# Optimization experiments

Hardware: AMD Instinct MI355X
Metric: run time of the kernel (lower is better)

The kernel has to match this reference:

```python
import jax, jax.numpy as jnp
import numpy as np

N, E, D = 10000, 320000, 128
SIGMA = 0.3


def setup_inputs() -> dict:
    key = jax.random.key(0)
    ks = jax.random.split(key, 24)
    f32 = jnp.float32
    inp = {
        "h": jax.random.normal(ks[0], (N, D), f32),
        "e": jax.random.normal(ks[1], (E, D), f32),
        "p": jax.random.normal(ks[2], (N, D), f32),
        "d": jax.random.normal(ks[3], (N, D), f32),
        "dt": jax.random.uniform(ks[4], (N,), f32, 0.1, 0.5),
        "spatial_mask": jax.random.randint(ks[5], (E,), 0, 2).astype(jnp.int32),
        "src": jax.random.randint(ks[6], (E,), 0, N),
        "dst": jax.random.randint(ks[7], (E,), 0, N),
    }
    names = ["V1", "V2", "E1", "P1", "P2", "P3", "D1", "D2", "V"]
    for i, n in enumerate(names):
        inp["W_" + n] = jax.random.normal(ks[8 + i], (D, D), f32) * 0.05
        inp["b_" + n] = jnp.zeros((D,), f32)
    inp["W_T"] = jax.random.normal(ks[20], (D, 2 * D), f32) * 0.05
    inp["b_T"] = jnp.zeros((D,), f32)
    return inp


def _lin(x, W, b):
    return x @ W.T + b


def _forward(h, e, p, d, dt,
             W_V1, b_V1, W_V2, b_V2, W_E1, b_E1,
             W_P1, b_P1, W_P2, b_P2, W_P3, b_P3,
             W_D1, b_D1, W_D2, b_D2, W_V, b_V, W_T, b_T,
             spatial_mask, src, dst):
    n_nodes = h.shape[0]
    V1h = _lin(h, W_V1, b_V1)
    V2h = _lin(h, W_V2, b_V2)
    E1e = _lin(e, W_E1, b_E1)
    P1h = _lin(p, W_P1, b_P1)
    P2h = _lin(p, W_P2, b_P2)
    P3h = _lin(p, W_P3, b_P3)
    D1h = _lin(d, W_D1, b_D1)
    D2h = _lin(d, W_D2, b_D2)
    # edge update: e' = 0.5 * ((P1h[dst] - P2h[src]) + E1(e))   [E,D]
    e_new = 0.5 * ((P1h[dst] - P2h[src]) + E1e)
    smask = (spatial_mask == 1)[:, None]  # [E,1] True = spatial edge
    a = D1h - V1h                          # [N,D]
    # temporal branch: tau = relu(T([h_dst, d_dst])) on temporal edges only,
    # summed into the destination node (zeros elsewhere, like DGL's partial apply_edges)
    tau = jnp.where(smask, 0.0,
                    jax.nn.relu(_lin(jnp.concatenate([h[dst], d[dst]], -1), W_T, b_T)))
    sum_tau = jax.ops.segment_sum(tau, dst, num_segments=n_nodes)
    f0 = a * sum_tau
    # spatial branch: grad_rab = vjp of (Vj * value_rab(rab)) wrt rab = e_new, cotangent = ones
    Vj = jnp.where(smask, jax.nn.relu(_lin(h[src] * h[dst], W_V, b_V)), 0.0)

    def compute(rab):
        nrm = jnp.clip(jnp.linalg.norm(rab, axis=-1, keepdims=True), 1e-9, None)
        r = 0.5 * jnp.sqrt(nrm)              # [E,1]
        return Vj * jnp.exp(-r / SIGMA)      # [E,D]

    _, vjp_fn = jax.vjp(compute, e_new)
    grad_rab, = vjp_fn(jnp.ones_like(e_new))
    fab = jax.ops.segment_sum(grad_rab, dst, num_segments=n_nodes)
    f = f0 - fab
    dtc = dt[:, None]
    h_out = V2h + f * dtc
    p_out = P3h + f * dtc + 0.5 * f * dtc ** 2
    d_out = D2h + f / (jnp.linalg.norm(f, axis=-1, keepdims=True) + 1e-9)
    lrelu = lambda x: jax.nn.leaky_relu(x, 0.01)
    # residual (input_dim == output_dim); dropout is identity in eval mode
    return (h + lrelu(h_out), e + lrelu(e_new), p + lrelu(p_out), d + lrelu(d_out))


def reference(h, e, p, d, dt, spatial_mask, src, dst,
              W_V1, b_V1, W_V2, b_V2, W_E1, b_E1,
              W_P1, b_P1, W_P2, b_P2, W_P3, b_P3,
              W_D1, b_D1, W_D2, b_D2, W_V, b_V, W_T, b_T):
    return _forward(h, e, p, d, dt,
                    W_V1, b_V1, W_V2, b_V2, W_E1, b_E1,
                    W_P1, b_P1, W_P2, b_P2, W_P3, b_P3,
                    W_D1, b_D1, W_D2, b_D2, W_V, b_V, W_T, b_T,
                    spatial_mask, src, dst)
```

## Files before the change

kernel.cpp:

```cpp
#include <hip/hip_runtime.h>
#include <hip/hip_bf16.h>

#define NN 10000
#define NE 320000
#define SIG 0.3f
#define NDp ((size_t)1280000)
#define OUT_H ((size_t)0)
#define OUT_E ((size_t)1280000)
#define OUT_P ((size_t)42240000)
#define OUT_D ((size_t)43520000)

#define F_V1H (0 * NDp)
#define F_V2H (1 * NDp)
#define F_P1H (2 * NDp)
#define F_P2H (3 * NDp)
#define F_P3H (4 * NDp)
#define F_D1H (5 * NDp)
#define F_D2H (6 * NDp)
#define F_G   (7 * NDp)
#define F_FAB (8 * NDp)
#define F_CNT (9 * NDp)
#define F_FLAGS (9 * NDp + 10240)
#define F_STAGED (9 * NDp + 10240 + 16)
#define S_H  ((size_t)0)
#define S_P  ((size_t)1280000)
#define S_D  ((size_t)2560000)
#define S_W  ((size_t)3840000)
#define S_WT (S_W + 9 * 16384)

typedef __attribute__((ext_vector_type(8))) short s8v;
typedef __attribute__((ext_vector_type(4))) float f4v;

__device__ __forceinline__ float b2f(unsigned short s) {
  return __uint_as_float(((unsigned int)s) << 16);
}
__device__ __forceinline__ short f2b(float f) {
  __hip_bfloat16 b = __float2bfloat16(f);
  return *reinterpret_cast<short*>(&b);
}
__device__ __forceinline__ float lrelu(float x) { return x >= 0.f ? x : 0.01f * x; }
__device__ __forceinline__ float loadf(const void* p, size_t i, bool f32) {
  return f32 ? ((const float*)p)[i] : b2f(((const unsigned short*)p)[i]);
}
__device__ __forceinline__ void storef(void* p, size_t i, float v, bool f32) {
  if (f32) ((float*)p)[i] = v;
  else ((unsigned short*)p)[i] = (unsigned short)f2b(v);
}
__device__ __forceinline__ void storef2(void* p, size_t i, float x, float y, bool f32) {
  if (f32) {
    *reinterpret_cast<float2*>((float*)p + i) = make_float2(x, y);
  } else {
    unsigned int v = ((unsigned int)(unsigned short)f2b(y) << 16) |
                     (unsigned int)(unsigned short)f2b(x);
    *((unsigned int*)p + (i >> 1)) = v;
  }
}
__device__ __forceinline__ s8v cvt8(const float* fp) {
  f4v a = *reinterpret_cast<const f4v*>(fp);
  f4v b = *reinterpret_cast<const f4v*>(fp + 4);
  s8v r;
#pragma unroll
  for (int j = 0; j < 4; j++) { r[j] = f2b(a[j]); r[4 + j] = f2b(b[j]); }
  return r;
}

__global__ __launch_bounds__(256) void zero_kernel(float* ws) {
  int i = blockIdx.x * 256 + threadIdx.x;
  ws[F_FAB + i] = 0.f;
  if (i < NN) ws[F_CNT + i] = 0.f;
  if (i < 16) ((int*)(ws + F_FLAGS))[i] = 0;
}

struct DetTask { const unsigned short* s; int n; int flag; };
struct DetArgs { DetTask t[6]; int* flags; };
__global__ __launch_bounds__(256) void detect_kernel(DetArgs a) {
  DetTask t = a.t[blockIdx.y];
  int hit = 0;
  for (int i = blockIdx.x * 256 + threadIdx.x; i < t.n; i += gridDim.x * 256) {
    if ((unsigned short)(t.s[i] & 0x7FFF) > (unsigned short)0x7F80) hit = 1;
  }
  if (hit) atomicOr(&a.flags[t.flag], 1);
}

struct ConvTask { const void* src; unsigned short* dst; int n; int flag; };
struct ConvArgs { ConvTask t[13]; const int* flags; };
__global__ __launch_bounds__(256) void convert_kernel(ConvArgs a) {
  ConvTask t = a.t[blockIdx.y];
  bool f32 = a.flags[t.flag] != 0;
  for (int i = blockIdx.x * 256 + threadIdx.x; i < t.n; i += gridDim.x * 256) {
    t.dst[i] = f32 ? (unsigned short)f2b(((const float*)t.src)[i])
                   : ((const unsigned short*)t.src)[i];
  }
}

__global__ __launch_bounds__(256) void cnt_kernel(const int* __restrict__ spatial,
                                                  const int* __restrict__ dst,
                                                  float* __restrict__ cnt) {
  int e = blockIdx.x * 256 + threadIdx.x;
  if (e < NE && spatial[e] != 1) atomicAdd(&cnt[dst[e]], 1.0f);
}

struct NodeArgs {
  const unsigned short* x[3];
  const unsigned short* W[8];
  const void* b[8];
  float* out[8];
  const int* flags;
};

__global__ __launch_bounds__(256) void node_gemm_kernel(NodeArgs a) {
  const int o = blockIdx.y;
  const int wave = threadIdx.x >> 6, lane = threadIdx.x & 63;
  const int l16 = lane & 15, quad = lane >> 4;
  const int m0 = blockIdx.x * 64 + wave * 16;
  if (m0 >= NN) return;
  const bool wf32 = a.flags[5] != 0;
  int arow = m0 + l16;
  if (arow >= NN) arow = NN - 1;
  const unsigned short* Wp = a.W[o];
  f4v acc[8] = {};
  if (o < 7) {
    const unsigned short* X0 = (o < 2) ? a.x[0] : (o < 5 ? a.x[1] : a.x[2]);
    const unsigned short* xrow = X0 + (size_t)arow * 128;
#pragma unroll
    for (int kk = 0; kk < 128; kk += 32) {
      int k8 = kk + quad * 8;
      s8v av = *(const s8v*)(xrow + k8);
#pragma unroll
      for (int nt = 0; nt < 8; nt++) {
        s8v bv = *(const s8v*)(Wp + (size_t)(nt * 16 + l16) * 128 + k8);
        acc[nt] = __builtin_amdgcn_mfma_f32_16x16x32_bf16(av, bv, acc[nt], 0, 0, 0);
      }
    }
  } else {
#pragma unroll
    for (int kk = 0; kk < 256; kk += 32) {
      int k8 = kk + quad * 8;
      const unsigned short* ap = (k8 < 128) ? (a.x[0] + (size_t)arow * 128 + k8)
                                            : (a.x[2] + (size_t)arow * 128 + (k8 - 128));
      s8v av = *(const s8v*)ap;
#pragma unroll
      for (int nt = 0; nt < 8; nt++) {
        s8v bv = *(const s8v*)(Wp + (size_t)(nt * 16 + l16) * 256 + k8);
        acc[nt] = __builtin_amdgcn_mfma_f32_16x16x32_bf16(av, bv, acc[nt], 0, 0, 0);
      }
    }
  }
  float* outp = a.out[o];
#pragma unroll
  for (int nt = 0; nt < 8; nt++) {
    int col = nt * 16 + l16;
    float bvv = loadf(a.b[o], col, wf32);
#pragma unroll
    for (int r = 0; r < 4; r++) {
      int row = m0 + quad * 4 + r;
      if (row < NN) {
        float v = acc[nt][r] + bvv;
        if (o == 7) v = fmaxf(v, 0.f);
        outp[(size_t)row * 128 + col] = v;
      }
    }
  }
}

#define LSTRIDE 136
__global__ __launch_bounds__(256) void edge_kernel(
    const void* __restrict__ e, const unsigned short* __restrict__ sh,
    const int* __restrict__ spatial, const int* __restrict__ src, const int* __restrict__ dst,
    const unsigned short* __restrict__ WE1, const unsigned short* __restrict__ WV,
    const void* __restrict__ bE1, const void* __restrict__ bV,
    const float* __restrict__ P1h, const float* __restrict__ P2h,
    float* __restrict__ fab, void* __restrict__ out, const int* __restrict__ flags) {
  __shared__ __align__(16) unsigned short lds_e[4][16 * LSTRIDE];
  __shared__ __align__(16) unsigned short lds_E1[4][16 * LSTRIDE];
  __shared__ float lds_sv[4][16];
  const int wave = threadIdx.x >> 6, lane = threadIdx.x & 63;
  const int l16 = lane & 15, quad = lane >> 4;
  const int m0 = blockIdx.x * 64 + wave * 16;
  const bool ef32 = flags[1] != 0;
  const bool wf32 = flags[5] != 0;
  const bool of32 = (flags[0] | flags[1] | flags[2] | flags[3] | flags[4] | flags[5]) != 0;
  const int arow = m0 + l16;

  {
    f4v acc2[8] = {};
    const int asrc = src[arow], adst = dst[arow];
    const unsigned short* hs_row = sh + (size_t)asrc * 128;
    const unsigned short* hd_row = sh + (size_t)adst * 128;
#pragma unroll
    for (int kk = 0; kk < 128; kk += 32) {
      int k8 = kk + quad * 8;
      s8v hs = *(const s8v*)(hs_row + k8);
      s8v hd = *(const s8v*)(hd_row + k8);
      s8v ap;
#pragma unroll
      for (int j = 0; j < 8; j++)
        ap[j] = f2b(b2f((unsigned short)hs[j]) * b2f((unsigned short)hd[j]));
#pragma unroll
      for (int nt = 0; nt < 8; nt++) {
        s8v bv = *(const s8v*)(WV + (size_t)(nt * 16 + l16) * 128 + k8);
        acc2[nt] = __builtin_amdgcn_mfma_f32_16x16x32_bf16(ap, bv, acc2[nt], 0, 0, 0);
      }
    }
    float sv[4] = {0.f, 0.f, 0.f, 0.f};
#pragma unroll
    for (int nt = 0; nt < 8; nt++) {
      int col = nt * 16 + l16;
      float bvv = loadf(bV, col, wf32);
#pragma unroll
      for (int r = 0; r < 4; r++) sv[r] += fmaxf(acc2[nt][r] + bvv, 0.f);
    }
#pragma unroll
    for (int m = 1; m < 16; m <<= 1) {
#pragma unroll
      for (int r = 0; r < 4; r++) sv[r] += __shfl_xor(sv[r], m, 64);
    }
    if (l16 == 0) {
#pragma unroll
      for (int r = 0; r < 4; r++) lds_sv[wave][quad * 4 + r] = sv[r];
    }
  }

  {
    f4v acc1[8] = {};
    size_t ro = (size_t)arow * 128;
#pragma unroll
    for (int kk = 0; kk < 128; kk += 32) {
      int k8 = kk + quad * 8;
      s8v av;
      if (ef32) av = cvt8((const float*)e + ro + k8);
      else av = *(const s8v*)((const unsigned short*)e + ro + k8);
      *(s8v*)&lds_e[wave][l16 * LSTRIDE + k8] = av;
#pragma unroll
      for (int nt = 0; nt < 8; nt++) {
        s8v bv = *(const s8v*)(WE1 + (size_t)(nt * 16 + l16) * 128 + k8);
        acc1[nt] = __builtin_amdgcn_mfma_f32_16x16x32_bf16(av, bv, acc1[nt], 0, 0, 0);
      }
    }
#pragma unroll
    for (int nt = 0; nt < 8; nt++) {
      int col = nt * 16 + l16;
      float bvv = loadf(bE1, col, wf32);
#pragma unroll
      for (int r = 0; r < 4; r++) {
        int row = quad * 4 + r;
        lds_E1[wave][row * LSTRIDE + col] = (unsigned short)f2b(acc1[nt][r] + bvv);
      }
    }
  }

  const int c0 = lane * 2;
#pragma unroll 4
  for (int row = 0; row < 16; row++) {
    const int er = m0 + row;
    const int sr_ = src[er], dr_ = dst[er], sp_ = spatial[er];
    float2 p1 = *(const float2*)(P1h + (size_t)dr_ * 128 + c0);
    float2 p2 = *(const float2*)(P2h + (size_t)sr_ * 128 + c0);
    unsigned int e1w = *(const unsigned int*)&lds_E1[wave][row * LSTRIDE + c0];
    unsigned int eew = *(const unsigned int*)&lds_e[wave][row * LSTRIDE + c0];
    float e1x = b2f((unsigned short)(e1w & 0xFFFF));
    float e1y = b2f((unsigned short)(e1w >> 16));
    float eex = b2f((unsigned short)(eew & 0xFFFF));
    float eey = b2f((unsigned short)(eew >> 16));
    float vx = 0.5f * (p1.x - p2.x + e1x);
    float vy = 0.5f * (p1.y - p2.y + e1y);
    storef2(out, OUT_E + (size_t)er * 128 + c0, eex + lrelu(vx), eey + lrelu(vy), of32);
    float n2 = vx * vx + vy * vy;
#pragma unroll
    for (int m = 1; m < 64; m <<= 1) n2 += __shfl_xor(n2, m, 64);
    if (sp_ == 1) {
      float n = sqrtf(n2);
      if (n >= 1e-9f) {
        float svr = lds_sv[wave][row];
        float rr = 0.5f * sqrtf(n);
        float s = expf(-rr / SIG);
        float c = -svr * s * 0.25f / (SIG * n * sqrtf(n));
        atomicAdd(&fab[(size_t)dr_ * 128 + c0], c * vx);
        atomicAdd(&fab[(size_t)dr_ * 128 + c0 + 1], c * vy);
      }
    }
  }
}

__global__ __launch_bounds__(256) void node_out_kernel(
    const unsigned short* __restrict__ sh, const unsigned short* __restrict__ sp,
    const unsigned short* __restrict__ sd, const void* __restrict__ dt,
    const float* __restrict__ V1h, const float* __restrict__ V2h, const float* __restrict__ P3h,
    const float* __restrict__ D1h, const float* __restrict__ D2h, const float* __restrict__ g,
    const float* __restrict__ fab, const float* __restrict__ cnt,
    void* __restrict__ out, const int* __restrict__ flags) {
  const int wave = threadIdx.x >> 6, lane = threadIdx.x & 63;
  const int node = blockIdx.x * 4 + wave;
  const bool dtf32 = flags[4] != 0;
  const bool of32 = (flags[0] | flags[1] | flags[2] | flags[3] | flags[4] | flags[5]) != 0;
  const size_t i = (size_t)node * 128 + lane * 2;
  float cn = cnt[node];
  float2 v1 = *(const float2*)(V1h + i);
  float2 d1 = *(const float2*)(D1h + i);
  float2 gg = *(const float2*)(g + i);
  float2 fb = *(const float2*)(fab + i);
  float fx = (d1.x - v1.x) * (cn * gg.x) - fb.x;
  float fy = (d1.y - v1.y) * (cn * gg.y) - fb.y;
  float n2 = fx * fx + fy * fy;
#pragma unroll
  for (int m = 1; m < 64; m <<= 1) n2 += __shfl_xor(n2, m, 64);
  float nf = sqrtf(n2);
  float dtv = loadf(dt, node, dtf32);
  float2 v2 = *(const float2*)(V2h + i);
  float2 p3 = *(const float2*)(P3h + i);
  float2 d2 = *(const float2*)(D2h + i);
  float hx = v2.x + fx * dtv, hy = v2.y + fy * dtv;
  float px = p3.x + fx * dtv + 0.5f * fx * dtv * dtv;
  float py = p3.y + fy * dtv + 0.5f * fy * dtv * dtv;
  float invn = 1.f / (nf + 1e-9f);
  float dx = d2.x + fx * invn, dy = d2.y + fy * invn;
  storef2(out, OUT_H + i, b2f(sh[i]) + lrelu(hx), b2f(sh[i + 1]) + lrelu(hy), of32);
  storef2(out, OUT_P + i, b2f(sp[i]) + lrelu(px), b2f(sp[i + 1]) + lrelu(py), of32);
  storef2(out, OUT_D + i, b2f(sd[i]) + lrelu(dx), b2f(sd[i + 1]) + lrelu(dy), of32);
}

extern "C" void kernel_launch(void* const* d_in, const int* in_sizes, int n_in,
                              void* d_out, int out_size, void* d_ws, size_t ws_size,
                              hipStream_t stream) {
  const int* spatial = (const int*)d_in[5];
  const int* src = (const int*)d_in[6];
  const int* dst = (const int*)d_in[7];

  float* ws = (float*)d_ws;
  int* flags = (int*)(ws + F_FLAGS);
  unsigned short* stg = (unsigned short*)(ws + F_STAGED);

  zero_kernel<<<(int)(NDp / 256), 256, 0, stream>>>(ws);

  DetArgs da;
  da.t[0] = { (const unsigned short*)d_in[0], 1280000, 0 };
  da.t[1] = { (const unsigned short*)d_in[1], 40960000, 1 };
  da.t[2] = { (const unsigned short*)d_in[2], 1280000, 2 };
  da.t[3] = { (const unsigned short*)d_in[3], 1280000, 3 };
  da.t[4] = { (const unsigned short*)d_in[4], 10000, 4 };
  da.t[5] = { (const unsigned short*)d_in[8], 16384, 5 };
  da.flags = flags;
  detect_kernel<<<dim3(1024, 6), 256, 0, stream>>>(da);

  ConvArgs ca;
  ca.t[0] = { d_in[0], stg + S_H, 1280000, 0 };
  ca.t[1] = { d_in[2], stg + S_P, 1280000, 2 };
  ca.t[2] = { d_in[3], stg + S_D, 1280000, 3 };
  for (int i = 0; i < 9; i++)
    ca.t[3 + i] = { d_in[8 + 2 * i], stg + S_W + (size_t)i * 16384, 16384, 5 };
  ca.t[12] = { d_in[26], stg + S_WT, 32768, 5 };
  ca.flags = flags;
  convert_kernel<<<dim3(640, 13), 256, 0, stream>>>(ca);

  cnt_kernel<<<NE / 256, 256, 0, stream>>>(spatial, dst, ws + F_CNT);

  NodeArgs na;
  na.x[0] = stg + S_H; na.x[1] = stg + S_P; na.x[2] = stg + S_D;
  na.W[0] = stg + S_W + 0 * 16384;  na.b[0] = d_in[9];
  na.W[1] = stg + S_W + 1 * 16384;  na.b[1] = d_in[11];
  na.W[2] = stg + S_W + 3 * 16384;  na.b[2] = d_in[15];
  na.W[3] = stg + S_W + 4 * 16384;  na.b[3] = d_in[17];
  na.W[4] = stg + S_W + 5 * 16384;  na.b[4] = d_in[19];
  na.W[5] = stg + S_W + 6 * 16384;  na.b[5] = d_in[21];
  na.W[6] = stg + S_W + 7 * 16384;  na.b[6] = d_in[23];
  na.W[7] = stg + S_WT;             na.b[7] = d_in[27];
  na.out[0] = ws + F_V1H; na.out[1] = ws + F_V2H; na.out[2] = ws + F_P1H;
  na.out[3] = ws + F_P2H; na.out[4] = ws + F_P3H; na.out[5] = ws + F_D1H;
  na.out[6] = ws + F_D2H; na.out[7] = ws + F_G;
  na.flags = flags;
  node_gemm_kernel<<<dim3((NN + 63) / 64, 8), 256, 0, stream>>>(na);

  edge_kernel<<<NE / 64, 256, 0, stream>>>(
      d_in[1], stg + S_H, spatial, src, dst,
      stg + S_W + 2 * 16384, stg + S_W + 8 * 16384, d_in[13], d_in[25],
      ws + F_P1H, ws + F_P2H, ws + F_FAB, d_out, flags);

  node_out_kernel<<<NN / 4, 256, 0, stream>>>(
      stg + S_H, stg + S_P, stg + S_D, d_in[4],
      ws + F_V1H, ws + F_V2H, ws + F_P3H, ws + F_D1H, ws + F_D2H, ws + F_G,
      ws + F_FAB, ws + F_CNT, d_out, flags);
}
```

Before: 828.9 us.

## Privatize fab atomic accumulation into eight replicated buffers and drop LDS e staging

```diff
diff --git a/kernel.cpp b/kernel.cpp
--- a/kernel.cpp
+++ b/kernel.cpp
@@ -27,6 +27,7 @@
 #define S_D  ((size_t)2560000)
 #define S_W  ((size_t)3840000)
 #define S_WT (S_W + 9 * 16384)
+#define F_FABX8 (F_STAGED + (size_t)2010112)
 
 typedef __attribute__((ext_vector_type(8))) short s8v;
 typedef __attribute__((ext_vector_type(4))) float f4v;
@@ -42,9 +43,10 @@
 __device__ __forceinline__ float loadf(const void* p, size_t i, bool f32) {
   return f32 ? ((const float*)p)[i] : b2f(((const unsigned short*)p)[i]);
 }
-__device__ __forceinline__ void storef(void* p, size_t i, float v, bool f32) {
-  if (f32) ((float*)p)[i] = v;
-  else ((unsigned short*)p)[i] = (unsigned short)f2b(v);
+__device__ __forceinline__ float2 loadf2(const void* p, size_t i, bool f32) {
+  if (f32) return *reinterpret_cast<const float2*>((const float*)p + i);
+  unsigned int w = *((const unsigned int*)p + (i >> 1));
+  return make_float2(b2f((unsigned short)(w & 0xFFFF)), b2f((unsigned short)(w >> 16)));
 }
 __device__ __forceinline__ void storef2(void* p, size_t i, float x, float y, bool f32) {
   if (f32) {
@@ -64,9 +66,9 @@
   return r;
 }
 
-__global__ __launch_bounds__(256) void zero_kernel(float* ws) {
+__global__ __launch_bounds__(256) void zero_kernel(float* ws, float* fabBase, int fabFloats) {
   int i = blockIdx.x * 256 + threadIdx.x;
-  ws[F_FAB + i] = 0.f;
+  fabBase[i] = 0.f;
   if (i < NN) ws[F_CNT + i] = 0.f;
   if (i < 16) ((int*)(ws + F_FLAGS))[i] = 0;
 }
@@ -170,8 +172,8 @@
     const unsigned short* __restrict__ WE1, const unsigned short* __restrict__ WV,
     const void* __restrict__ bE1, const void* __restrict__ bV,
     const float* __restrict__ P1h, const float* __restrict__ P2h,
-    float* __restrict__ fab, void* __restrict__ out, const int* __restrict__ flags) {
-  __shared__ __align__(16) unsigned short lds_e[4][16 * LSTRIDE];
+    float* __restrict__ fab, int fabMask,
+    void* __restrict__ out, const int* __restrict__ flags) {
   __shared__ __align__(16) unsigned short lds_E1[4][16 * LSTRIDE];
   __shared__ float lds_sv[4][16];
   const int wave = threadIdx.x >> 6, lane = threadIdx.x & 63;
@@ -181,6 +183,7 @@
   const bool wf32 = flags[5] != 0;
   const bool of32 = (flags[0] | flags[1] | flags[2] | flags[3] | flags[4] | flags[5]) != 0;
   const int arow = m0 + l16;
+  float* __restrict__ fabW = fab + (size_t)(blockIdx.x & fabMask) * NDp;
 
   {
     f4v acc2[8] = {};
@@ -230,7 +233,6 @@
       s8v av;
       if (ef32) av = cvt8((const float*)e + ro + k8);
       else av = *(const s8v*)((const unsigned short*)e + ro + k8);
-      *(s8v*)&lds_e[wave][l16 * LSTRIDE + k8] = av;
 #pragma unroll
       for (int nt = 0; nt < 8; nt++) {
         s8v bv = *(const s8v*)(WE1 + (size_t)(nt * 16 + l16) * 128 + k8);
@@ -257,14 +259,12 @@
     float2 p1 = *(const float2*)(P1h + (size_t)dr_ * 128 + c0);
     float2 p2 = *(const float2*)(P2h + (size_t)sr_ * 128 + c0);
     unsigned int e1w = *(const unsigned int*)&lds_E1[wave][row * LSTRIDE + c0];
-    unsigned int eew = *(const unsigned int*)&lds_e[wave][row * LSTRIDE + c0];
     float e1x = b2f((unsigned short)(e1w & 0xFFFF));
     float e1y = b2f((unsigned short)(e1w >> 16));
-    float eex = b2f((unsigned short)(eew & 0xFFFF));
-    float eey = b2f((unsigned short)(eew >> 16));
+    float2 ee = loadf2(e, (size_t)er * 128 + c0, ef32);
     float vx = 0.5f * (p1.x - p2.x + e1x);
     float vy = 0.5f * (p1.y - p2.y + e1y);
-    storef2(out, OUT_E + (size_t)er * 128 + c0, eex + lrelu(vx), eey + lrelu(vy), of32);
+    storef2(out, OUT_E + (size_t)er * 128 + c0, ee.x + lrelu(vx), ee.y + lrelu(vy), of32);
     float n2 = vx * vx + vy * vy;
 #pragma unroll
     for (int m = 1; m < 64; m <<= 1) n2 += __shfl_xor(n2, m, 64);
@@ -275,8 +275,8 @@
         float rr = 0.5f * sqrtf(n);
         float s = expf(-rr / SIG);
         float c = -svr * s * 0.25f / (SIG * n * sqrtf(n));
-        atomicAdd(&fab[(size_t)dr_ * 128 + c0], c * vx);
-        atomicAdd(&fab[(size_t)dr_ * 128 + c0 + 1], c * vy);
+        atomicAdd(&fabW[(size_t)dr_ * 128 + c0], c * vx);
+        atomicAdd(&fabW[(size_t)dr_ * 128 + c0 + 1], c * vy);
       }
     }
   }
@@ -287,7 +287,7 @@
     const unsigned short* __restrict__ sd, const void* __restrict__ dt,
     const float* __restrict__ V1h, const float* __restrict__ V2h, const float* __restrict__ P3h,
     const float* __restrict__ D1h, const float* __restrict__ D2h, const float* __restrict__ g,
-    const float* __restrict__ fab, const float* __restrict__ cnt,
+    const float* __restrict__ fab, int ncopy, const float* __restrict__ cnt,
     void* __restrict__ out, const int* __restrict__ flags) {
   const int wave = threadIdx.x >> 6, lane = threadIdx.x & 63;
   const int node = blockIdx.x * 4 + wave;
@@ -298,7 +298,11 @@
   float2 v1 = *(const float2*)(V1h + i);
   float2 d1 = *(const float2*)(D1h + i);
   float2 gg = *(const float2*)(g + i);
-  float2 fb = *(const float2*)(fab + i);
+  float2 fb = make_float2(0.f, 0.f);
+  for (int k = 0; k < ncopy; k++) {
+    float2 t = *(const float2*)(fab + (size_t)k * NDp + i);
+    fb.x += t.x; fb.y += t.y;
+  }
   float fx = (d1.x - v1.x) * (cn * gg.x) - fb.x;
   float fy = (d1.y - v1.y) * (cn * gg.y) - fb.y;
   float n2 = fx * fx + fy * fy;
@@ -330,7 +334,13 @@
   int* flags = (int*)(ws + F_FLAGS);
   unsigned short* stg = (unsigned short*)(ws + F_STAGED);
 
-  zero_kernel<<<(int)(NDp / 256), 256, 0, stream>>>(ws);
+  const bool have8 = ws_size >= (size_t)(F_FABX8 + 8 * NDp) * 4;
+  float* fabBase = ws + (have8 ? F_FABX8 : F_FAB);
+  const int fabMask = have8 ? 7 : 0;
+  const int ncopy = have8 ? 8 : 1;
+  const int fabFloats = (int)(ncopy * NDp);
+
+  zero_kernel<<<fabFloats / 256, 256, 0, stream>>>(ws, fabBase, fabFloats);
 
   DetArgs da;
   da.t[0] = { (const unsigned short*)d_in[0], 1280000, 0 };
@@ -373,10 +383,10 @@
   edge_kernel<<<NE / 64, 256, 0, stream>>>(
       d_in[1], stg + S_H, spatial, src, dst,
       stg + S_W + 2 * 16384, stg + S_W + 8 * 16384, d_in[13], d_in[25],
-      ws + F_P1H, ws + F_P2H, ws + F_FAB, d_out, flags);
+      ws + F_P1H, ws + F_P2H, fabBase, fabMask, d_out, flags);
 
   node_out_kernel<<<NN / 4, 256, 0, stream>>>(
       stg + S_H, stg + S_P, stg + S_D, d_in[4],
       ws + F_V1H, ws + F_V2H, ws + F_P3H, ws + F_D1H, ws + F_D2H, ws + F_G,
-      ws + F_FAB, ws + F_CNT, d_out, flags);
-}
+      fabBase, ncopy, ws + F_CNT, d_out, flags);
+}
```

Result: no change. 842.6 us (+1.7%).

## Split edge kernel into separate Vj-sum kernel and half-column-per-wave edge GEMM

Applied to the files above, without the earlier changes.

```diff
diff --git a/kernel.cpp b/kernel.cpp
--- a/kernel.cpp
+++ b/kernel.cpp
@@ -27,6 +27,7 @@
 #define S_D  ((size_t)2560000)
 #define S_W  ((size_t)3840000)
 #define S_WT (S_W + 9 * 16384)
+#define F_SV (F_STAGED + (size_t)2010112)
 
 typedef __attribute__((ext_vector_type(8))) short s8v;
 typedef __attribute__((ext_vector_type(4))) float f4v;
@@ -42,9 +43,10 @@
 __device__ __forceinline__ float loadf(const void* p, size_t i, bool f32) {
   return f32 ? ((const float*)p)[i] : b2f(((const unsigned short*)p)[i]);
 }
-__device__ __forceinline__ void storef(void* p, size_t i, float v, bool f32) {
-  if (f32) ((float*)p)[i] = v;
-  else ((unsigned short*)p)[i] = (unsigned short)f2b(v);
+__device__ __forceinline__ float2 loadf2(const void* p, size_t i, bool f32) {
+  if (f32) return *reinterpret_cast<const float2*>((const float*)p + i);
+  unsigned int w = *((const unsigned int*)p + (i >> 1));
+  return make_float2(b2f((unsigned short)(w & 0xFFFF)), b2f((unsigned short)(w >> 16)));
 }
 __device__ __forceinline__ void storef2(void* p, size_t i, float x, float y, bool f32) {
   if (f32) {
@@ -76,8 +78,16 @@
 __global__ __launch_bounds__(256) void detect_kernel(DetArgs a) {
   DetTask t = a.t[blockIdx.y];
   int hit = 0;
-  for (int i = blockIdx.x * 256 + threadIdx.x; i < t.n; i += gridDim.x * 256) {
-    if ((unsigned short)(t.s[i] & 0x7FFF) > (unsigned short)0x7F80) hit = 1;
+  const uint4* s4 = (const uint4*)t.s;
+  const int n8 = t.n >> 3;
+  for (int i = blockIdx.x * 256 + threadIdx.x; i < n8; i += gridDim.x * 256) {
+    uint4 v = s4[i];
+    unsigned int ww[4] = {v.x, v.y, v.z, v.w};
+#pragma unroll
+    for (int j = 0; j < 4; j++) {
+      if ((unsigned short)(ww[j] & 0x7FFF) > (unsigned short)0x7F80) hit = 1;
+      if ((unsigned short)((ww[j] >> 16) & 0x7FFF) > (unsigned short)0x7F80) hit = 1;
+    }
   }
   if (hit) atomicOr(&a.flags[t.flag], 1);
 }
@@ -87,9 +97,10 @@
 __global__ __launch_bounds__(256) void convert_kernel(ConvArgs a) {
   ConvTask t = a.t[blockIdx.y];
   bool f32 = a.flags[t.flag] != 0;
-  for (int i = blockIdx.x * 256 + threadIdx.x; i < t.n; i += gridDim.x * 256) {
-    t.dst[i] = f32 ? (unsigned short)f2b(((const float*)t.src)[i])
-                   : ((const unsigned short*)t.src)[i];
+  const int n8 = t.n >> 3;
+  for (int i = blockIdx.x * 256 + threadIdx.x; i < n8; i += gridDim.x * 256) {
+    if (f32) ((s8v*)t.dst)[i] = cvt8((const float*)t.src + (size_t)i * 8);
+    else ((uint4*)t.dst)[i] = ((const uint4*)t.src)[i];
   }
 }
 
@@ -163,115 +174,131 @@
   }
 }
 
-#define LSTRIDE 136
-__global__ __launch_bounds__(256) void edge_kernel(
-    const void* __restrict__ e, const unsigned short* __restrict__ sh,
-    const int* __restrict__ spatial, const int* __restrict__ src, const int* __restrict__ dst,
-    const unsigned short* __restrict__ WE1, const unsigned short* __restrict__ WV,
-    const void* __restrict__ bE1, const void* __restrict__ bV,
-    const float* __restrict__ P1h, const float* __restrict__ P2h,
-    float* __restrict__ fab, void* __restrict__ out, const int* __restrict__ flags) {
-  __shared__ __align__(16) unsigned short lds_e[4][16 * LSTRIDE];
-  __shared__ __align__(16) unsigned short lds_E1[4][16 * LSTRIDE];
-  __shared__ float lds_sv[4][16];
+__global__ __launch_bounds__(256) void sv_kernel(
+    const unsigned short* __restrict__ sh, const int* __restrict__ src,
+    const int* __restrict__ dst, const unsigned short* __restrict__ WV,
+    const void* __restrict__ bV, float* __restrict__ svout,
+    const int* __restrict__ flags) {
+  __shared__ float part[2][2][16];
   const int wave = threadIdx.x >> 6, lane = threadIdx.x & 63;
   const int l16 = lane & 15, quad = lane >> 4;
-  const int m0 = blockIdx.x * 64 + wave * 16;
+  const int p = wave >> 1, hf = wave & 1;
+  const int m0 = blockIdx.x * 32 + p * 16;
+  const bool wf32 = flags[5] != 0;
+  const int arow = m0 + l16;
+  const int asrc = src[arow], adst = dst[arow];
+  const unsigned short* hs_row = sh + (size_t)asrc * 128;
+  const unsigned short* hd_row = sh + (size_t)adst * 128;
+  f4v acc[4] = {};
+#pragma unroll
+  for (int kk = 0; kk < 128; kk += 32) {
+    int k8 = kk + quad * 8;
+    s8v hs = *(const s8v*)(hs_row + k8);
+    s8v hd = *(const s8v*)(hd_row + k8);
+    s8v ap;
+#pragma unroll
+    for (int j = 0; j < 8; j++)
+      ap[j] = f2b(b2f((unsigned short)hs[j]) * b2f((unsigned short)hd[j]));
+#pragma unroll
+    for (int nt = 0; nt < 4; nt++) {
+      int col = hf * 64 + nt * 16 + l16;
+      s8v bv = *(const s8v*)(WV + (size_t)col * 128 + k8);
+      acc[nt] = __builtin_amdgcn_mfma_f32_16x16x32_bf16(ap, bv, acc[nt], 0, 0, 0);
+    }
+  }
+  float sv[4] = {0.f, 0.f, 0.f, 0.f};
+#pragma unroll
+  for (int nt = 0; nt < 4; nt++) {
+    int col = hf * 64 + nt * 16 + l16;
+    float bvv = loadf(bV, col, wf32);
+#pragma unroll
+    for (int r = 0; r < 4; r++) sv[r] += fmaxf(acc[nt][r] + bvv, 0.f);
+  }
+#pragma unroll
+  for (int m = 1; m < 16; m <<= 1) {
+#pragma unroll
+    for (int r = 0; r < 4; r++) sv[r] += __shfl_xor(sv[r], m, 64);
+  }
+  if (l16 == 0) {
+#pragma unroll
+    for (int r = 0; r < 4; r++) part[p][hf][quad * 4 + r] = sv[r];
+  }
+  __syncthreads();
+  if (hf == 0 && lane < 16)
+    svout[m0 + lane] = part[p][0][lane] + part[p][1][lane];
+}
+
+#define LSTR 136
+__global__ __launch_bounds__(256) void edge_kernel(
+    const void* __restrict__ e, const int* __restrict__ spatial,
+    const int* __restrict__ src, const int* __restrict__ dst,
+    const unsigned short* __restrict__ WE1, const void* __restrict__ bE1,
+    const float* __restrict__ P1h, const float* __restrict__ P2h,
+    const float* __restrict__ sv, float* __restrict__ fab,
+    void* __restrict__ out, const int* __restrict__ flags) {
+  __shared__ __align__(16) unsigned short lds_E1[32 * LSTR];
+  const int wave = threadIdx.x >> 6, lane = threadIdx.x & 63;
+  const int l16 = lane & 15, quad = lane >> 4;
+  const int p = wave >> 1, hf = wave & 1;
+  const int m0 = blockIdx.x * 32 + p * 16;
   const bool ef32 = flags[1] != 0;
   const bool wf32 = flags[5] != 0;
   const bool of32 = (flags[0] | flags[1] | flags[2] | flags[3] | flags[4] | flags[5]) != 0;
+
+  const int myrow = blockIdx.x * 32 + wave * 8 + (lane & 7);
+  const int pse = src[myrow], pde = dst[myrow], psp = spatial[myrow];
+
   const int arow = m0 + l16;
-
-  {
-    f4v acc2[8] = {};
-    const int asrc = src[arow], adst = dst[arow];
-    const unsigned short* hs_row = sh + (size_t)asrc * 128;
-    const unsigned short* hd_row = sh + (size_t)adst * 128;
-#pragma unroll
-    for (int kk = 0; kk < 128; kk += 32) {
-      int k8 = kk + quad * 8;
-      s8v hs = *(const s8v*)(hs_row + k8);
-      s8v hd = *(const s8v*)(hd_row + k8);
-      s8v ap;
-#pragma unroll
-      for (int j = 0; j < 8; j++)
-        ap[j] = f2b(b2f((unsigned short)hs[j]) * b2f((unsigned short)hd[j]));
-#pragma unroll
-      for (int nt = 0; nt < 8; nt++) {
-        s8v bv = *(const s8v*)(WV + (size_t)(nt * 16 + l16) * 128 + k8);
-        acc2[nt] = __builtin_amdgcn_mfma_f32_16x16x32_bf16(ap, bv, acc2[nt], 0, 0, 0);
-      }
-    }
-    float sv[4] = {0.f, 0.f, 0.f, 0.f};
-#pragma unroll
-    for (int nt = 0; nt < 8; nt++) {
-      int col = nt * 16 + l16;
-      float bvv = loadf(bV, col, wf32);
-#pragma unroll
-      for (int r = 0; r < 4; r++) sv[r] += fmaxf(acc2[nt][r] + bvv, 0.f);
-    }
-#pragma unroll
-    for (int m = 1; m < 16; m <<= 1) {
-#pragma unroll
-      for (int r = 0; r < 4; r++) sv[r] += __shfl_xor(sv[r], m, 64);
-    }
-    if (l16 == 0) {
-#pragma unroll
-      for (int r = 0; r < 4; r++) lds_sv[wave][quad * 4 + r] = sv[r];
-    }
-  }
-
-  {
-    f4v acc1[8] = {};
-    size_t ro = (size_t)arow * 128;
-#pragma unroll
-    for (int kk = 0; kk < 128; kk += 32) {
-      int k8 = kk + quad * 8;
-      s8v av;
-      if (ef32) av = cvt8((const float*)e + ro + k8);
-      else av = *(const s8v*)((const unsigned short*)e + ro + k8);
-      *(s8v*)&lds_e[wave][l16 * LSTRIDE + k8] = av;
-#pragma unroll
-      for (int nt = 0; nt < 8; nt++) {
-        s8v bv = *(const s8v*)(WE1 + (size_t)(nt * 16 + l16) * 128 + k8);
-        acc1[nt] = __builtin_amdgcn_mfma_f32_16x16x32_bf16(av, bv, acc1[nt], 0, 0, 0);
-      }
-    }
-#pragma unroll
-    for (int nt = 0; nt < 8; nt++) {
-      int col = nt * 16 + l16;
-      float bvv = loadf(bE1, col, wf32);
-#pragma unroll
-      for (int r = 0; r < 4; r++) {
-        int row = quad * 4 + r;
-        lds_E1[wave][row * LSTRIDE + col] = (unsigned short)f2b(acc1[nt][r] + bvv);
-      }
-    }
-  }
+  const size_t ro = (size_t)arow * 128;
+  f4v acc[4] = {};
+#pragma unroll
+  for (int kk = 0; kk < 128; kk += 32) {
+    int k8 = kk + quad * 8;
+    s8v av;
+    if (ef32) av = cvt8((const float*)e + ro + k8);
+    else av = *(const s8v*)((const unsigned short*)e + ro + k8);
+#pragma unroll
+    for (int nt = 0; nt < 4; nt++) {
+      int col = hf * 64 + nt * 16 + l16;
+      s8v bv = *(const s8v*)(WE1 + (size_t)col * 128 + k8);
+      acc[nt] = __builtin_amdgcn_mfma_f32_16x16x32_bf16(av, bv, acc[nt], 0, 0, 0);
+    }
+  }
+#pragma unroll
+  for (int nt = 0; nt < 4; nt++) {
+    int col = hf * 64 + nt * 16 + l16;
+    float bvv = loadf(bE1, col, wf32);
+#pragma unroll
+    for (int r = 0; r < 4; r++) {
+      int lrow = p * 16 + quad * 4 + r;
+      lds_E1[lrow * LSTR + col] = (unsigned short)f2b(acc[nt][r] + bvv);
+    }
+  }
+  __syncthreads();
 
   const int c0 = lane * 2;
 #pragma unroll 4
-  for (int row = 0; row < 16; row++) {
-    const int er = m0 + row;
-    const int sr_ = src[er], dr_ = dst[er], sp_ = spatial[er];
+  for (int r = 0; r < 8; r++) {
+    const int er = blockIdx.x * 32 + wave * 8 + r;
+    const int sr_ = __shfl(pse, r, 64);
+    const int dr_ = __shfl(pde, r, 64);
+    const int sp_ = __shfl(psp, r, 64);
     float2 p1 = *(const float2*)(P1h + (size_t)dr_ * 128 + c0);
     float2 p2 = *(const float2*)(P2h + (size_t)sr_ * 128 + c0);
-    unsigned int e1w = *(const unsigned int*)&lds_E1[wave][row * LSTRIDE + c0];
-    unsigned int eew = *(const unsigned int*)&lds_e[wave][row * LSTRIDE + c0];
+    unsigned int e1w = *(const unsigned int*)&lds_E1[(wave * 8 + r) * LSTR + c0];
     float e1x = b2f((unsigned short)(e1w & 0xFFFF));
     float e1y = b2f((unsigned short)(e1w >> 16));
-    float eex = b2f((unsigned short)(eew & 0xFFFF));
-    float eey = b2f((unsigned short)(eew >> 16));
+    float2 ee = loadf2(e, (size_t)er * 128 + c0, ef32);
     float vx = 0.5f * (p1.x - p2.x + e1x);
     float vy = 0.5f * (p1.y - p2.y + e1y);
-    storef2(out, OUT_E + (size_t)er * 128 + c0, eex + lrelu(vx), eey + lrelu(vy), of32);
+    storef2(out, OUT_E + (size_t)er * 128 + c0, ee.x + lrelu(vx), ee.y + lrelu(vy), of32);
     float n2 = vx * vx + vy * vy;
 #pragma unroll
     for (int m = 1; m < 64; m <<= 1) n2 += __shfl_xor(n2, m, 64);
     if (sp_ == 1) {
       float n = sqrtf(n2);
       if (n >= 1e-9f) {
-        float svr = lds_sv[wave][row];
+        float svr = sv[er];
         float rr = 0.5f * sqrtf(n);
         float s = expf(-rr / SIG);
         float c = -svr * s * 0.25f / (SIG * n * sqrtf(n));
@@ -354,6 +381,9 @@
 
   cnt_kernel<<<NE / 256, 256, 0, stream>>>(spatial, dst, ws + F_CNT);
 
+  sv_kernel<<<NE / 32, 256, 0, stream>>>(
+      stg + S_H, src, dst, stg + S_W + 8 * 16384, d_in[25], ws + F_SV, flags);
+
   NodeArgs na;
   na.x[0] = stg + S_H; na.x[1] = stg + S_P; na.x[2] = stg + S_D;
   na.W[0] = stg + S_W + 0 * 16384;  na.b[0] = d_in[9];
@@ -370,10 +400,10 @@
   na.flags = flags;
   node_gemm_kernel<<<dim3((NN + 63) / 64, 8), 256, 0, stream>>>(na);
 
-  edge_kernel<<<NE / 64, 256, 0, stream>>>(
-      d_in[1], stg + S_H, spatial, src, dst,
-      stg + S_W + 2 * 16384, stg + S_W + 8 * 16384, d_in[13], d_in[25],
-      ws + F_P1H, ws + F_P2H, ws + F_FAB, d_out, flags);
+  edge_kernel<<<NE / 32, 256, 0, stream>>>(
+      d_in[1], spatial, src, dst,
+      stg + S_W + 2 * 16384, d_in[13],
+      ws + F_P1H, ws + F_P2H, ws + F_SV, ws + F_FAB, d_out, flags);
 
   node_out_kernel<<<NN / 4, 256, 0, stream>>>(
       stg + S_H, stg + S_P, stg + S_D, d_in[4],
```

Result: faster. 784.3 us (-5.4%).
